# Optimization experiments

Measured on AMD Instinct MI355X. Metric: run time of the kernel, lower is better.

Reference implementation:

```python
import jax, jax.numpy as jnp
import numpy as np

# ---- static config ----
G = 4          # num graphs
NG = 512       # nodes per graph
N = G * NG     # total nodes
E = 32768      # num edges
IN_DIM = 128
HID = 32
HEADS = 4
HC = HID * HEADS  # 128
OUT_DIM = 32
N_LAYERS = 2
GRID = 500
Q = 20
NEG_SLOPE = 0.2
QUANTILES = jnp.asarray(np.linspace(0.0, 1.0, Q), jnp.float32)  # [Q]


def setup_inputs() -> dict:
    key = jax.random.key(0)
    ks = jax.random.split(key, 32)
    inp = {}
    inp['x'] = jax.random.normal(ks[0], (N, IN_DIM), jnp.float32)
    inp['edge_index'] = jax.random.randint(ks[1], (2, E), 0, N).astype(jnp.int64)
    inp['batch'] = (jnp.arange(N) // NG).astype(jnp.int64)
    # GATConv params (2 layers, both 128 -> 4 heads x 32, concat)
    for l, (kin,) in enumerate([(IN_DIM,), (HC,)]):
        s = 1.0 / np.sqrt(kin)
        inp[f'W{l}'] = jax.random.normal(ks[2 + 4 * l], (kin, HC), jnp.float32) * s
        inp[f'as{l}'] = jax.random.normal(ks[3 + 4 * l], (HEADS, HID), jnp.float32) * s
        inp[f'ad{l}'] = jax.random.normal(ks[4 + 4 * l], (HEADS, HID), jnp.float32) * s
        inp[f'b{l}'] = jnp.zeros((HC,), jnp.float32)
    for l in range(N_LAYERS + 1):
        inp[f'lpW{l}'] = jax.random.normal(ks[10 + 2 * l], (HC, OUT_DIM), jnp.float32) * (1.0 / np.sqrt(HC))
        inp[f'lpb{l}'] = jnp.zeros((OUT_DIM,), jnp.float32)
    for l in range(N_LAYERS + 1):
        inp[f'kW{l}'] = jax.random.normal(ks[16 + 2 * l], (HC * Q, OUT_DIM), jnp.float32) * (1.0 / np.sqrt(HC * Q))
        inp[f'kb{l}'] = jnp.zeros((OUT_DIM,), jnp.float32)
    inp['pool_w'] = jnp.ones((2,), jnp.float32) / 2.0
    inp['beta'] = jax.random.normal(ks[22], (OUT_DIM,), jnp.float32)
    inp['h0'] = jax.random.normal(ks[23], (1,), jnp.float32)
    return inp


def _gat_layer(x, src, dst, W, a_src, a_dst, bias):
    # PyG GATConv (concat=True, add_self_loops=True, negative_slope=0.2), eval mode
    n = x.shape[0]
    xh = (x @ W).reshape(n, HEADS, HID)              # [N,H,C]
    loop = jnp.arange(n)
    s = jnp.concatenate([src, loop])                 # [E+N]
    d = jnp.concatenate([dst, loop])
    al_s = jnp.einsum('nhc,hc->nh', xh, a_src)       # [N,H]
    al_d = jnp.einsum('nhc,hc->nh', xh, a_dst)
    e = jax.nn.leaky_relu(al_s[s] + al_d[d], NEG_SLOPE)   # [E+N,H]
    e_max = jax.ops.segment_max(e, d, num_segments=n)     # stable softmax per dst
    e = jnp.exp(e - e_max[d])
    denom = jax.ops.segment_sum(e, d, num_segments=n)
    alpha = e / (denom[d] + 1e-16)                   # [E+N,H]
    out = jax.ops.segment_sum(alpha[:, :, None] * xh[s], d, num_segments=n)
    return out.reshape(n, HC) + bias


def _kde_per_graph(xg):
    # xg: [Ng, D] -> [D*Q] soft-quantile features via grid KDE
    n = xg.shape[0]
    mn = xg.min(axis=0) - 1e-6                       # [D]
    mx = xg.max(axis=0) + 1e-6
    grid = jnp.linspace(0.0, 1.0, GRID)[:, None] * (mx - mn) + mn   # [Gp,D]
    std = xg.std(axis=0) + 1e-8 / 3
    h = 1.06 * std * float(n) ** (-0.2)              # [D]
    u = (grid[:, None, :] - xg[None, :, :]) / h      # [Gp,Ng,D]  (dominant tensor)
    kern = jnp.exp(-0.5 * u * u) / (h * np.sqrt(2.0 * np.pi))
    density = kern.mean(axis=1)                      # [Gp,D]
    cdf = jnp.cumsum(density, axis=0)
    cdf = cdf / jnp.clip(cdf[-1:], 1e-8)
    dist = jnp.abs(cdf[:, :, None] - QUANTILES)      # [Gp,D,Q]
    w = jax.nn.sigmoid(-100.0 * dist)
    w = w / (w.sum(axis=0, keepdims=True) + 1e-8)
    qv = (grid[:, :, None] * w).sum(axis=0)          # [D,Q]
    return qv.reshape(-1)


def _readout(cur, lpW, lpb, kW, kb, pool_w):
    xr = cur.reshape(G, NG, -1)
    pooled = jnp.stack([xr.mean(axis=1), xr.max(axis=1)], axis=0)   # [2,G,D]
    wp = (pooled * pool_w[:, None, None]).sum(axis=0)               # [G,D]
    h = wp @ lpW + lpb                                              # [G,out]
    kf = jax.vmap(_kde_per_graph)(xr)                               # [G,D*Q]
    return h, kf @ kW + kb


def reference(x, edge_index, batch, W0, as0, ad0, b0, W1, as1, ad1, b1,
              lpW0, lpb0, lpW1, lpb1, lpW2, lpb2,
              kW0, kb0, kW1, kb1, kW2, kb2, pool_w, beta, h0):
    src, dst = edge_index[0], edge_index[1]
    convs = [(W0, as0, ad0, b0), (W1, as1, ad1, b1)]
    lps = [(lpW0, lpb0), (lpW1, lpb1), (lpW2, lpb2)]
    kps = [(kW0, kb0), (kW1, kb1), (kW2, kb2)]
    cur = x
    h_list, kde_list = [], []
    for i in range(N_LAYERS):
        h, kp = _readout(cur, lps[i][0], lps[i][1], kps[i][0], kps[i][1], pool_w)
        h_list.append(h); kde_list.append(kp)
        cur = _gat_layer(cur, src, dst, *convs[i])
        if i != N_LAYERS - 1:
            cur = jax.nn.relu(cur)
    h, kp = _readout(cur, lps[-1][0], lps[-1][1], kps[-1][0], kps[-1][1], pool_w)
    h_list.append(h); kde_list.append(kp)
    main_out = jnp.stack(h_list).mean(axis=0)        # [G,out]
    kde_out = jnp.stack(kde_list).mean(axis=0)
    risk = (main_out + kde_out) @ beta + h0          # [G]
    return risk
```

## Files before the change

kernel.cpp:

```cpp
#include <hip/hip_runtime.h>
#include <math.h>

#define GNUM 4
#define NG 512
#define NN 2048
#define EE 32768
#define HC 128
#define HEADS 4
#define HID 32
#define GRID_PTS 500
#define QN 20
#define ODIM 32
#define MAXE 160

#define LOG2E 1.44269504088896340736f
#define NEG_HALF_LOG2E -0.72134752044448170368f
#define N_POW_M02 0.2871745887492588f
#define SIG_K 144.269504089f

__device__ __forceinline__ float fexp2(float x){ return __builtin_amdgcn_exp2f(x); }
__device__ __forceinline__ float frcp(float x){ return __builtin_amdgcn_rcpf(x); }

struct SmemKDE {
  __align__(16) float2 xs[NG];
  float4 wred4[8];
  float sc[4];
  float wsum[8], woff[9];
  float redw[QN][8], redg[QN][8];
  float qs[QN];
};
struct SmemXW  { float rows[4][HC]; };
struct SmemGat {
  int   ssrc[4][MAXE];
  float sexp[4][MAXE][HEADS];
  float smax[4][HEADS], sfac[4][HEADS];
};
union Smem { SmemKDE kde; SmemXW xw; SmemGat gat; };

__device__ void kde_phase(Smem& sm, const float* __restrict__ cur, int do_relu, int trans,
        const float* __restrict__ kW, const float* __restrict__ kb,
        const float* __restrict__ lpW, const float* __restrict__ lpb,
        const float* __restrict__ poolw, const float* __restrict__ beta,
        float* __restrict__ outg){
  int b = blockIdx.x;
  int g = b >> 7, d = b & 127;
  int t = threadIdx.x;
  int lane = t & 63, wave = t >> 6;
  float v = trans ? cur[(size_t)d*NN + g*NG + t]
                  : cur[((size_t)g*NG + t)*HC + d];
  if (do_relu) v = fmaxf(v, 0.f);
  sm.kde.xs[t] = make_float2(v, v*v);
  float mn=v, mx=v, smv=v, sq=v*v;
  #pragma unroll
  for (int m=32; m>0; m>>=1){
    mn = fminf(mn, __shfl_xor(mn, m, 64));
    mx = fmaxf(mx, __shfl_xor(mx, m, 64));
    smv += __shfl_xor(smv, m, 64);
    sq += __shfl_xor(sq, m, 64);
  }
  if (lane==0) sm.kde.wred4[wave] = make_float4(mn,mx,smv,sq);
  __syncthreads();
  if (t==0){
    float4 r = sm.kde.wred4[0];
    #pragma unroll
    for (int i=1;i<8;++i){
      float4 bb = sm.kde.wred4[i];
      r.x = fminf(r.x,bb.x); r.y = fmaxf(r.y,bb.y); r.z += bb.z; r.w += bb.w;
    }
    float mean = r.z * (1.f/NG);
    float var  = fmaxf(r.w*(1.f/NG) - mean*mean, 0.f);
    float sd   = sqrtf(var) + (1e-8f/3.f);
    float h    = 1.06f * sd * N_POW_M02;
    float lo = r.x - 1e-6f, hi = r.y + 1e-6f;
    sm.kde.sc[0] = lo;
    sm.kde.sc[1] = (hi-lo)*(1.f/(GRID_PTS-1));
    sm.kde.sc[2] = NEG_HALF_LOG2E/(h*h);
    sm.kde.sc[3] = poolw[0]*mean + poolw[1]*r.y;
  }
  __syncthreads();
  float lo = sm.kde.sc[0], st = sm.kde.sc[1], kk = sm.kde.sc[2];
  float gv = lo + st*(float)t;
  float acc = 0.f;
  if (t < GRID_PTS){
    float c0 = kk*gv*gv, c1 = -2.f*kk*gv;
    const float4* p4 = (const float4*)sm.kde.xs;
    #pragma unroll 4
    for (int i=0;i<NG/2;++i){
      float4 s2 = p4[i];
      acc += fexp2(fmaf(kk, s2.y, fmaf(c1, s2.x, c0)));
      acc += fexp2(fmaf(kk, s2.w, fmaf(c1, s2.z, c0)));
    }
  }
  float sv = acc;
  #pragma unroll
  for (int off=1; off<64; off<<=1){
    float n = __shfl_up(sv, off, 64);
    if (lane >= off) sv += n;
  }
  if (lane==63) sm.kde.wsum[wave] = sv;
  __syncthreads();
  if (t==0){
    float r2 = 0.f;
    #pragma unroll
    for (int i=0;i<8;++i){ sm.kde.woff[i]=r2; r2+=sm.kde.wsum[i]; }
    sm.kde.woff[8]=r2;
  }
  if (t < QN*8){ ((float*)sm.kde.redw)[t]=0.f; ((float*)sm.kde.redg)[t]=0.f; }
  __syncthreads();
  float invt = 1.f/fmaxf(sm.kde.woff[8], 1e-8f);
  float c = (sv + sm.kde.woff[wave]) * invt;
  float cw0 = __shfl(c, 0, 64), cw1 = __shfl(c, 63, 64);
  int qlo = max(0, (int)ceilf((cw0 - 0.17f)*(float)(QN-1)));
  int qhi = min(QN-1, (int)floorf((cw1 + 0.17f)*(float)(QN-1)));
  for (int q=qlo; q<=qhi; ++q){
    float w = 0.f;
    if (t < GRID_PTS){
      float dist = fabsf(c - (float)q*(1.f/(QN-1)));
      w = frcp(1.f + fexp2(SIG_K*dist));
    }
    float gw = gv*w;
    #pragma unroll
    for (int m=32;m>0;m>>=1){
      w  += __shfl_xor(w,  m, 64);
      gw += __shfl_xor(gw, m, 64);
    }
    if (lane==0){ sm.kde.redw[q][wave]=w; sm.kde.redg[q][wave]=gw; }
  }
  __syncthreads();
  if (t < QN){
    float sw=0.f, sgw=0.f;
    #pragma unroll
    for (int i=0;i<8;++i){ sw+=sm.kde.redw[t][i]; sgw+=sm.kde.redg[t][i]; }
    sm.kde.qs[t] = sgw / (sw + 1e-8f);
  }
  __syncthreads();
  if (t < ODIM){
    float a = 0.f;
    const float* kwb = kW + (size_t)d*QN*ODIM + t;
    #pragma unroll
    for (int q=0;q<QN;++q) a += sm.kde.qs[q]*kwb[q*ODIM];
    if (d==0) a += kb[t];
    float bb = sm.kde.sc[3]*lpW[d*ODIM + t];
    if (d==0) bb += lpb[t];
    float s = beta[t]*(a + bb);
    #pragma unroll
    for (int m=16;m>0;m>>=1) s += __shfl_xor(s, m, 32);
    if (t==0) atomicAdd(&outg[g], s*(1.f/3.f));
  }
  __syncthreads();
}

__device__ float gather_core(Smem& sm, int d, int sub, int tl,
        const int* __restrict__ csr, const int* __restrict__ pos,
        const float* __restrict__ als, const float* __restrict__ ald,
        const float* __restrict__ xh, const float* __restrict__ bias){
  int deg = min(pos[d], MAXE-1);
  int E = deg + 1;
  const int* base = csr + d*MAXE;
  float a0 = ald[d*4+0], a1 = ald[d*4+1], a2 = ald[d*4+2], a3 = ald[d*4+3];
  for (int i=tl; i<E; i+=128){
    int s = (i < deg) ? base[i] : d;
    sm.gat.ssrc[sub][i] = s;
    float e0 = als[s*4+0]+a0, e1 = als[s*4+1]+a1, e2 = als[s*4+2]+a2, e3 = als[s*4+3]+a3;
    e0 = (e0>=0.f)? e0 : 0.2f*e0;
    e1 = (e1>=0.f)? e1 : 0.2f*e1;
    e2 = (e2>=0.f)? e2 : 0.2f*e2;
    e3 = (e3>=0.f)? e3 : 0.2f*e3;
    sm.gat.sexp[sub][i][0]=e0; sm.gat.sexp[sub][i][1]=e1;
    sm.gat.sexp[sub][i][2]=e2; sm.gat.sexp[sub][i][3]=e3;
  }
  __syncthreads();
  if (tl < HEADS){
    float m = -INFINITY;
    for (int i=0;i<E;++i) m = fmaxf(m, sm.gat.sexp[sub][i][tl]);
    sm.gat.smax[sub][tl] = m;
  }
  __syncthreads();
  for (int i=tl; i<E; i+=128){
    #pragma unroll
    for (int h=0;h<HEADS;++h)
      sm.gat.sexp[sub][i][h] = fexp2(LOG2E*(sm.gat.sexp[sub][i][h]-sm.gat.smax[sub][h]));
  }
  __syncthreads();
  if (tl < HEADS){
    float sdn = 0.f;
    for (int i=0;i<E;++i) sdn += sm.gat.sexp[sub][i][tl];
    sm.gat.sfac[sub][tl] = 1.f/(sdn + 1e-16f);
  }
  __syncthreads();
  int h = tl >> 5;
  float fac = sm.gat.sfac[sub][h];
  float acc = bias[tl];
  for (int i=0;i<E;++i)
    acc += sm.gat.sexp[sub][i][h]*fac * xh[(size_t)sm.gat.ssrc[sub][i]*HC + tl];
  __syncthreads();
  return acc;
}

__device__ void xw_emit(Smem& sm, int sub, int j, int n,
        const float* __restrict__ W, const float* __restrict__ as_, const float* __restrict__ ad_,
        float* __restrict__ xh, float* __restrict__ als, float* __restrict__ ald){
  float acc = 0.f;
  #pragma unroll 8
  for (int c2=0;c2<HC;++c2)
    acc += sm.xw.rows[sub][c2]*W[(size_t)c2*HC + j];
  xh[(size_t)n*HC + j] = acc;
  int h = j >> 5, cc = j & 31;
  float ps = acc*as_[h*HID+cc], pd = acc*ad_[h*HID+cc];
  #pragma unroll
  for (int m=16;m>0;m>>=1){
    ps += __shfl_xor(ps, m, 32);
    pd += __shfl_xor(pd, m, 32);
  }
  if (cc==0){ als[n*HEADS+h]=ps; ald[n*HEADS+h]=pd; }
}

__device__ void write_transposed(Smem& sm, int t, int n0, float* __restrict__ curT){
  if (t < HC){
    float4 v = make_float4(sm.xw.rows[0][t], sm.xw.rows[1][t],
                           sm.xw.rows[2][t], sm.xw.rows[3][t]);
    *(float4*)(curT + (size_t)t*NN + n0) = v;
  }
}

__global__ __launch_bounds__(1024) void k_zero(int* __restrict__ pos,
        float* __restrict__ outg, const float* __restrict__ h0){
  int t = threadIdx.x;
  pos[t] = 0; pos[t+1024] = 0;
  if (t < GNUM) outg[t] = h0[0];
}

__global__ __launch_bounds__(512) void k_L0(const float* __restrict__ x,
        const float* __restrict__ kW, const float* __restrict__ kb,
        const float* __restrict__ lpW, const float* __restrict__ lpb,
        const float* __restrict__ poolw, const float* __restrict__ beta,
        float* __restrict__ outg,
        const float* __restrict__ W, const float* __restrict__ as_, const float* __restrict__ ad_,
        float* __restrict__ xh, float* __restrict__ als, float* __restrict__ ald,
        const int* __restrict__ src, const int* __restrict__ dst,
        int* __restrict__ pos, int* __restrict__ csr){
  __shared__ Smem sm;
  int t = threadIdx.x;
  if (blockIdx.x < 512){
    kde_phase(sm, x, 0, 0, kW, kb, lpW, lpb, poolw, beta, outg);
  } else {
    int b2 = blockIdx.x - 512;
    if (t < 64){
      int e = b2*64 + t;
      int dd = dst[e];
      int pp = atomicAdd(&pos[dd], 1);
      if (pp < MAXE) csr[dd*MAXE + pp] = src[e];
    }
    int sub = t >> 7, j = t & 127;
    int n = b2*4 + sub;
    sm.xw.rows[sub][j] = x[(size_t)n*HC + j];
    __syncthreads();
    xw_emit(sm, sub, j, n, W, as_, ad_, xh, als, ald);
  }
}

__global__ __launch_bounds__(512) void k_G0(const int* __restrict__ csr, const int* __restrict__ pos,
        const float* __restrict__ als_in, const float* __restrict__ ald_in,
        const float* __restrict__ xh_in, const float* __restrict__ bias,
        float* __restrict__ cur1T,
        const float* __restrict__ W1, const float* __restrict__ as1, const float* __restrict__ ad1,
        float* __restrict__ xh2, float* __restrict__ als2, float* __restrict__ ald2){
  __shared__ Smem sm;
  int t = threadIdx.x;
  int sub = t >> 7, tl = t & 127;
  int d = blockIdx.x*4 + sub;
  float acc = gather_core(sm, d, sub, tl, csr, pos, als_in, ald_in, xh_in, bias);
  sm.xw.rows[sub][tl] = fmaxf(acc, 0.f);
  __syncthreads();
  write_transposed(sm, t, blockIdx.x*4, cur1T);
  xw_emit(sm, sub, tl, d, W1, as1, ad1, xh2, als2, ald2);
}

__global__ __launch_bounds__(512) void k_L1(const float* __restrict__ cur1T,
        const float* __restrict__ kW, const float* __restrict__ kb,
        const float* __restrict__ lpW, const float* __restrict__ lpb,
        const float* __restrict__ poolw, const float* __restrict__ beta,
        float* __restrict__ outg,
        const int* __restrict__ csr, const int* __restrict__ pos,
        const float* __restrict__ als2, const float* __restrict__ ald2,
        const float* __restrict__ xh2, const float* __restrict__ bias,
        float* __restrict__ cur2T){
  __shared__ Smem sm;
  int t = threadIdx.x;
  if (blockIdx.x < 512){
    kde_phase(sm, cur1T, 0, 1, kW, kb, lpW, lpb, poolw, beta, outg);
  } else {
    int b2 = blockIdx.x - 512;
    int sub = t >> 7, tl = t & 127;
    int d = b2*4 + sub;
    float acc = gather_core(sm, d, sub, tl, csr, pos, als2, ald2, xh2, bias);
    sm.xw.rows[sub][tl] = acc;
    __syncthreads();
    write_transposed(sm, t, b2*4, cur2T);
  }
}

__global__ __launch_bounds__(512) void k_L2(const float* __restrict__ cur2T,
        const float* __restrict__ kW, const float* __restrict__ kb,
        const float* __restrict__ lpW, const float* __restrict__ lpb,
        const float* __restrict__ poolw, const float* __restrict__ beta,
        float* __restrict__ outg){
  __shared__ Smem sm;
  kde_phase(sm, cur2T, 0, 1, kW, kb, lpW, lpb, poolw, beta, outg);
}

extern "C" void kernel_launch(void* const* d_in, const int* in_sizes, int n_in,
                              void* d_out, int out_size, void* d_ws, size_t ws_size,
                              hipStream_t stream) {
  (void)in_sizes; (void)n_in; (void)out_size; (void)ws_size;
  const float* x    = (const float*)d_in[0];
  const int*   ei   = (const int*)d_in[1];
  const int*   srcp = ei;
  const int*   dstp = ei + EE;
  const float* W[2]   = {(const float*)d_in[3], (const float*)d_in[7]};
  const float* As[2]  = {(const float*)d_in[4], (const float*)d_in[8]};
  const float* Ad[2]  = {(const float*)d_in[5], (const float*)d_in[9]};
  const float* Bi[2]  = {(const float*)d_in[6], (const float*)d_in[10]};
  const float* lpW[3] = {(const float*)d_in[11], (const float*)d_in[13], (const float*)d_in[15]};
  const float* lpb[3] = {(const float*)d_in[12], (const float*)d_in[14], (const float*)d_in[16]};
  const float* kW[3]  = {(const float*)d_in[17], (const float*)d_in[19], (const float*)d_in[21]};
  const float* kb[3]  = {(const float*)d_in[18], (const float*)d_in[20], (const float*)d_in[22]};
  const float* poolw  = (const float*)d_in[23];
  const float* beta   = (const float*)d_in[24];
  const float* h0     = (const float*)d_in[25];
  float* out = (float*)d_out;

  float* ws = (float*)d_ws;
  float* cur1T = ws;
  float* cur2T = cur1T + 262144;
  float* xh    = cur2T + 262144;
  float* xh2   = xh + 262144;
  float* als   = xh2 + 262144;
  float* ald   = als + 8192;
  float* als2  = ald + 8192;
  float* ald2  = als2 + 8192;
  int*   pos   = (int*)(ald2 + 8192);
  int*   csr   = pos + 2048;

  k_zero<<<1, 1024, 0, stream>>>(pos, out, h0);
  k_L0<<<1024, 512, 0, stream>>>(x, kW[0], kb[0], lpW[0], lpb[0], poolw, beta, out,
                                 W[0], As[0], Ad[0], xh, als, ald,
                                 srcp, dstp, pos, csr);
  k_G0<<<512, 512, 0, stream>>>(csr, pos, als, ald, xh, Bi[0], cur1T,
                                W[1], As[1], Ad[1], xh2, als2, ald2);
  k_L1<<<1024, 512, 0, stream>>>(cur1T, kW[1], kb[1], lpW[1], lpb[1], poolw, beta, out,
                                 csr, pos, als2, ald2, xh2, Bi[1], cur2T);
  k_L2<<<512, 512, 0, stream>>>(cur2T, kW[2], kb[2], lpW[2], lpb[2], poolw, beta, out);
}
```

Before: 203.7 us.

## Split KDE into density and quantile phases and overlap them with GAT stages

The KDE readout is split into a density phase and a quantile phase that run as separate kernels. In the density phase each (graph, dim) pair is handled by two blocks, each summing half of the 512 samples; partial densities and stats go to global scratch. The quantile phase reads them back and is co-scheduled with the next GAT gather, or with the next layer's density phase. This gives more parallelism to the exp-heavy density loop and spreads work more evenly across launches. The cost is extra global traffic for the partial densities, one more launch, and the stats being computed twice per pair.

```diff
diff --git a/kernel.cpp b/kernel.cpp
--- a/kernel.cpp
+++ b/kernel.cpp
@@ -37,18 +37,15 @@
 };
 union Smem { SmemKDE kde; SmemXW xw; SmemGat gat; };
 
-__device__ void kde_phase(Smem& sm, const float* __restrict__ cur, int do_relu, int trans,
-        const float* __restrict__ kW, const float* __restrict__ kb,
-        const float* __restrict__ lpW, const float* __restrict__ lpb,
-        const float* __restrict__ poolw, const float* __restrict__ beta,
-        float* __restrict__ outg){
-  int b = blockIdx.x;
-  int g = b >> 7, d = b & 127;
+__device__ void dens_phase(Smem& sm, int db, const float* __restrict__ cur, int trans,
+        const float* __restrict__ poolw,
+        float4* __restrict__ gstats, float* __restrict__ gdens){
+  int gd = db >> 1, half = db & 1;
+  int g = gd >> 7, d = gd & 127;
   int t = threadIdx.x;
   int lane = t & 63, wave = t >> 6;
   float v = trans ? cur[(size_t)d*NN + g*NG + t]
                   : cur[((size_t)g*NG + t)*HC + d];
-  if (do_relu) v = fmaxf(v, 0.f);
   sm.kde.xs[t] = make_float2(v, v*v);
   float mn=v, mx=v, smv=v, sq=v*v;
   #pragma unroll
@@ -72,10 +69,11 @@
     float sd   = sqrtf(var) + (1e-8f/3.f);
     float h    = 1.06f * sd * N_POW_M02;
     float lo = r.x - 1e-6f, hi = r.y + 1e-6f;
-    sm.kde.sc[0] = lo;
-    sm.kde.sc[1] = (hi-lo)*(1.f/(GRID_PTS-1));
-    sm.kde.sc[2] = NEG_HALF_LOG2E/(h*h);
-    sm.kde.sc[3] = poolw[0]*mean + poolw[1]*r.y;
+    float stp = (hi-lo)*(1.f/(GRID_PTS-1));
+    float kk  = NEG_HALF_LOG2E/(h*h);
+    float pooled = poolw[0]*mean + poolw[1]*r.y;
+    sm.kde.sc[0] = lo; sm.kde.sc[1] = stp; sm.kde.sc[2] = kk;
+    if (half==0) gstats[gd] = make_float4(lo, stp, kk, pooled);
   }
   __syncthreads();
   float lo = sm.kde.sc[0], st = sm.kde.sc[1], kk = sm.kde.sc[2];
@@ -84,13 +82,31 @@
   if (t < GRID_PTS){
     float c0 = kk*gv*gv, c1 = -2.f*kk*gv;
     const float4* p4 = (const float4*)sm.kde.xs;
+    int i0 = half*128;
     #pragma unroll 4
-    for (int i=0;i<NG/2;++i){
+    for (int i=i0; i<i0+128; ++i){
       float4 s2 = p4[i];
       acc += fexp2(fmaf(kk, s2.y, fmaf(c1, s2.x, c0)));
       acc += fexp2(fmaf(kk, s2.w, fmaf(c1, s2.z, c0)));
     }
-  }
+    gdens[gd*1024 + half*512 + t] = acc;
+  }
+}
+
+__device__ void quant_phase(Smem& sm, int gd,
+        const float4* __restrict__ gstats, const float* __restrict__ gdens,
+        const float* __restrict__ kW, const float* __restrict__ kb,
+        const float* __restrict__ lpW, const float* __restrict__ lpb,
+        const float* __restrict__ beta, float* __restrict__ outg){
+  int g = gd >> 7, d = gd & 127;
+  int t = threadIdx.x;
+  int lane = t & 63, wave = t >> 6;
+  float4 stq = gstats[gd];
+  float lo = stq.x, st = stq.y, pooled = stq.w;
+  float acc = 0.f;
+  if (t < GRID_PTS)
+    acc = gdens[gd*1024 + t] + gdens[gd*1024 + 512 + t];
+  float gv = lo + st*(float)t;
   float sv = acc;
   #pragma unroll
   for (int off=1; off<64; off<<=1){
@@ -140,14 +156,13 @@
     #pragma unroll
     for (int q=0;q<QN;++q) a += sm.kde.qs[q]*kwb[q*ODIM];
     if (d==0) a += kb[t];
-    float bb = sm.kde.sc[3]*lpW[d*ODIM + t];
+    float bb = pooled*lpW[d*ODIM + t];
     if (d==0) bb += lpb[t];
     float s = beta[t]*(a + bb);
     #pragma unroll
     for (int m=16;m>0;m>>=1) s += __shfl_xor(s, m, 32);
     if (t==0) atomicAdd(&outg[g], s*(1.f/3.f));
   }
-  __syncthreads();
 }
 
 __device__ float gather_core(Smem& sm, int d, int sub, int tl,
@@ -230,21 +245,18 @@
   if (t < GNUM) outg[t] = h0[0];
 }
 
-__global__ __launch_bounds__(512) void k_L0(const float* __restrict__ x,
-        const float* __restrict__ kW, const float* __restrict__ kb,
-        const float* __restrict__ lpW, const float* __restrict__ lpb,
-        const float* __restrict__ poolw, const float* __restrict__ beta,
-        float* __restrict__ outg,
+__global__ __launch_bounds__(512) void k_A(const float* __restrict__ x,
+        const float* __restrict__ poolw, float4* __restrict__ gstatsA, float* __restrict__ gdensA,
         const float* __restrict__ W, const float* __restrict__ as_, const float* __restrict__ ad_,
         float* __restrict__ xh, float* __restrict__ als, float* __restrict__ ald,
         const int* __restrict__ src, const int* __restrict__ dst,
         int* __restrict__ pos, int* __restrict__ csr){
   __shared__ Smem sm;
   int t = threadIdx.x;
-  if (blockIdx.x < 512){
-    kde_phase(sm, x, 0, 0, kW, kb, lpW, lpb, poolw, beta, outg);
+  if (blockIdx.x < 1024){
+    dens_phase(sm, blockIdx.x, x, 0, poolw, gstatsA, gdensA);
   } else {
-    int b2 = blockIdx.x - 512;
+    int b2 = blockIdx.x - 1024;
     if (t < 64){
       int e = b2*64 + t;
       int dd = dst[e];
@@ -259,54 +271,76 @@
   }
 }
 
-__global__ __launch_bounds__(512) void k_G0(const int* __restrict__ csr, const int* __restrict__ pos,
-        const float* __restrict__ als_in, const float* __restrict__ ald_in,
-        const float* __restrict__ xh_in, const float* __restrict__ bias,
+__global__ __launch_bounds__(512) void k_B(const float4* __restrict__ gstatsA,
+        const float* __restrict__ gdensA,
+        const float* __restrict__ kW0, const float* __restrict__ kb0,
+        const float* __restrict__ lpW0, const float* __restrict__ lpb0,
+        const float* __restrict__ beta, float* __restrict__ outg,
+        const int* __restrict__ csr, const int* __restrict__ pos,
+        const float* __restrict__ als, const float* __restrict__ ald,
+        const float* __restrict__ xh, const float* __restrict__ Bi0,
         float* __restrict__ cur1T,
         const float* __restrict__ W1, const float* __restrict__ as1, const float* __restrict__ ad1,
         float* __restrict__ xh2, float* __restrict__ als2, float* __restrict__ ald2){
   __shared__ Smem sm;
   int t = threadIdx.x;
-  int sub = t >> 7, tl = t & 127;
-  int d = blockIdx.x*4 + sub;
-  float acc = gather_core(sm, d, sub, tl, csr, pos, als_in, ald_in, xh_in, bias);
-  sm.xw.rows[sub][tl] = fmaxf(acc, 0.f);
-  __syncthreads();
-  write_transposed(sm, t, blockIdx.x*4, cur1T);
-  xw_emit(sm, sub, tl, d, W1, as1, ad1, xh2, als2, ald2);
-}
-
-__global__ __launch_bounds__(512) void k_L1(const float* __restrict__ cur1T,
-        const float* __restrict__ kW, const float* __restrict__ kb,
-        const float* __restrict__ lpW, const float* __restrict__ lpb,
-        const float* __restrict__ poolw, const float* __restrict__ beta,
-        float* __restrict__ outg,
-        const int* __restrict__ csr, const int* __restrict__ pos,
-        const float* __restrict__ als2, const float* __restrict__ ald2,
-        const float* __restrict__ xh2, const float* __restrict__ bias,
-        float* __restrict__ cur2T){
-  __shared__ Smem sm;
-  int t = threadIdx.x;
   if (blockIdx.x < 512){
-    kde_phase(sm, cur1T, 0, 1, kW, kb, lpW, lpb, poolw, beta, outg);
+    quant_phase(sm, blockIdx.x, gstatsA, gdensA, kW0, kb0, lpW0, lpb0, beta, outg);
   } else {
     int b2 = blockIdx.x - 512;
     int sub = t >> 7, tl = t & 127;
-    int d = b2*4 + sub;
-    float acc = gather_core(sm, d, sub, tl, csr, pos, als2, ald2, xh2, bias);
+    int d2 = b2*4 + sub;
+    float acc = gather_core(sm, d2, sub, tl, csr, pos, als, ald, xh, Bi0);
+    sm.xw.rows[sub][tl] = fmaxf(acc, 0.f);
+    __syncthreads();
+    write_transposed(sm, t, b2*4, cur1T);
+    xw_emit(sm, sub, tl, d2, W1, as1, ad1, xh2, als2, ald2);
+  }
+}
+
+__global__ __launch_bounds__(512) void k_C(const float* __restrict__ cur1T,
+        const float* __restrict__ poolw, float4* __restrict__ gstatsB, float* __restrict__ gdensB,
+        const int* __restrict__ csr, const int* __restrict__ pos,
+        const float* __restrict__ als2, const float* __restrict__ ald2,
+        const float* __restrict__ xh2, const float* __restrict__ Bi1,
+        float* __restrict__ cur2T){
+  __shared__ Smem sm;
+  int t = threadIdx.x;
+  if (blockIdx.x < 1024){
+    dens_phase(sm, blockIdx.x, cur1T, 1, poolw, gstatsB, gdensB);
+  } else {
+    int b2 = blockIdx.x - 1024;
+    int sub = t >> 7, tl = t & 127;
+    int d2 = b2*4 + sub;
+    float acc = gather_core(sm, d2, sub, tl, csr, pos, als2, ald2, xh2, Bi1);
     sm.xw.rows[sub][tl] = acc;
     __syncthreads();
     write_transposed(sm, t, b2*4, cur2T);
   }
 }
 
-__global__ __launch_bounds__(512) void k_L2(const float* __restrict__ cur2T,
-        const float* __restrict__ kW, const float* __restrict__ kb,
-        const float* __restrict__ lpW, const float* __restrict__ lpb,
-        const float* __restrict__ poolw, const float* __restrict__ beta,
-        float* __restrict__ outg){
-  __shared__ Smem sm;
-  kde_phase(sm, cur2T, 0, 1, kW, kb, lpW, lpb, poolw, beta, outg);
+__global__ __launch_bounds__(512) void k_D(const float4* __restrict__ gstatsB,
+        const float* __restrict__ gdensB,
+        const float* __restrict__ kW1, const float* __restrict__ kb1,
+        const float* __restrict__ lpW1, const float* __restrict__ lpb1,
+        const float* __restrict__ beta, float* __restrict__ outg,
+        const float* __restrict__ cur2T, const float* __restrict__ poolw,
+        float4* __restrict__ gstatsA, float* __restrict__ gdensA){
+  __shared__ Smem sm;
+  if (blockIdx.x < 512){
+    quant_phase(sm, blockIdx.x, gstatsB, gdensB, kW1, kb1, lpW1, lpb1, beta, outg);
+  } else {
+    dens_phase(sm, blockIdx.x - 512, cur2T, 1, poolw, gstatsA, gdensA);
+  }
+}
+
+__global__ __launch_bounds__(512) void k_E(const float4* __restrict__ gstatsA,
+        const float* __restrict__ gdensA,
+        const float* __restrict__ kW2, const float* __restrict__ kb2,
+        const float* __restrict__ lpW2, const float* __restrict__ lpb2,
+        const float* __restrict__ beta, float* __restrict__ outg){
+  __shared__ Smem sm;
+  quant_phase(sm, blockIdx.x, gstatsA, gdensA, kW2, kb2, lpW2, lpb2, beta, outg);
 }
 
 extern "C" void kernel_launch(void* const* d_in, const int* in_sizes, int n_in,
@@ -331,24 +365,31 @@
   float* out = (float*)d_out;
 
   float* ws = (float*)d_ws;
-  float* cur1T = ws;
-  float* cur2T = cur1T + 262144;
-  float* xh    = cur2T + 262144;
-  float* xh2   = xh + 262144;
-  float* als   = xh2 + 262144;
-  float* ald   = als + 8192;
-  float* als2  = ald + 8192;
-  float* ald2  = als2 + 8192;
-  int*   pos   = (int*)(ald2 + 8192);
-  int*   csr   = pos + 2048;
+  float* cur1T  = ws;
+  float* cur2T  = cur1T + 262144;
+  float* xh     = cur2T + 262144;
+  float* xh2    = xh + 262144;
+  float* als    = xh2 + 262144;
+  float* ald    = als + 8192;
+  float* als2   = ald + 8192;
+  float* ald2   = als2 + 8192;
+  float* gdensA = ald2 + 8192;
+  float* gdensB = gdensA + 524288;
+  float4* gstatsA = (float4*)(gdensB + 524288);
+  float4* gstatsB = gstatsA + 512;
+  int*   pos    = (int*)(gstatsB + 512);
+  int*   csr    = pos + 2048;
 
   k_zero<<<1, 1024, 0, stream>>>(pos, out, h0);
-  k_L0<<<1024, 512, 0, stream>>>(x, kW[0], kb[0], lpW[0], lpb[0], poolw, beta, out,
-                                 W[0], As[0], Ad[0], xh, als, ald,
-                                 srcp, dstp, pos, csr);
-  k_G0<<<512, 512, 0, stream>>>(csr, pos, als, ald, xh, Bi[0], cur1T,
+  k_A<<<1536, 512, 0, stream>>>(x, poolw, gstatsA, gdensA,
+                                W[0], As[0], Ad[0], xh, als, ald,
+                                srcp, dstp, pos, csr);
+  k_B<<<1024, 512, 0, stream>>>(gstatsA, gdensA, kW[0], kb[0], lpW[0], lpb[0], beta, out,
+                                csr, pos, als, ald, xh, Bi[0], cur1T,
                                 W[1], As[1], Ad[1], xh2, als2, ald2);
-  k_L1<<<1024, 512, 0, stream>>>(cur1T, kW[1], kb[1], lpW[1], lpb[1], poolw, beta, out,
-                                 csr, pos, als2, ald2, xh2, Bi[1], cur2T);
-  k_L2<<<512, 512, 0, stream>>>(cur2T, kW[2], kb[2], lpW[2], lpb[2], poolw, beta, out);
-}
+  k_C<<<1536, 512, 0, stream>>>(cur1T, poolw, gstatsB, gdensB,
+                                csr, pos, als2, ald2, xh2, Bi[1], cur2T);
+  k_D<<<1536, 512, 0, stream>>>(gstatsB, gdensB, kW[1], kb[1], lpW[1], lpb[1], beta, out,
+                                cur2T, poolw, gstatsA, gdensA);
+  k_E<<<512, 512, 0, stream>>>(gstatsA, gdensA, kW[2], kb[2], lpW[2], lpb[2], beta, out);
+}
```

Measured after the change: 210.3 us. +3.2%, slower.
